# Optimization experiments

Hardware: AMD Instinct MI355X
Metric: run time of the kernel (lower is better)

Reference implementation:

```python
import jax, jax.numpy as jnp
import numpy as np

B, N, E, D, H = 1, 100000, 3200000, 16, 128
EPS = 1e-5


def _layer_norm(x, g, b):
    m = jnp.mean(x, axis=-1, keepdims=True)
    v = jnp.mean((x - m) ** 2, axis=-1, keepdims=True)
    return (x - m) * jax.lax.rsqrt(v + EPS) * g + b


def setup_inputs() -> dict:
    key = jax.random.key(0)
    ks = jax.random.split(key, 12)
    inp = {
        "nodes": jax.random.normal(ks[0], (B, N, D), dtype=jnp.float32),
        "edges": jax.random.randint(ks[1], (B, E, 2), 0, N, dtype=jnp.int32),
        "edge_weights": jax.random.uniform(ks[2], (B, E), dtype=jnp.float32),
    }
    dims = [(3 * D, H), (H, H), (H, H), (H, D)]
    for i, (din, dout) in enumerate(dims, start=1):
        inp[f"W{i}"] = jax.random.normal(ks[2 + i], (din, dout), dtype=jnp.float32) * (1.0 / np.sqrt(din))
        inp[f"b{i}"] = jnp.zeros((dout,), dtype=jnp.float32)
        inp[f"g{i}"] = jnp.ones((dout,), dtype=jnp.float32)
        inp[f"be{i}"] = jnp.zeros((dout,), dtype=jnp.float32)
    return inp


def reference(nodes, edges, edge_weights,
              W1, b1, g1, be1, W2, b2, g2, be2,
              W3, b3, g3, be3, W4, b4, g4, be4):
    src = edges[..., 0]  # [B,E]
    dst = edges[..., 1]
    w = edge_weights[..., None]  # [B,E,1]
    # edge-weighted endpoint features
    msg_in = jnp.take_along_axis(nodes, src[..., None], axis=1) * w   # [B,E,D]
    msg_out = jnp.take_along_axis(nodes, dst[..., None], axis=1) * w  # [B,E,D]
    # per-node sum aggregation (scatter-add over edge lists)
    b_idx = jnp.arange(B)[:, None]
    agg_in = jnp.zeros_like(nodes).at[b_idx, dst].add(msg_in)   # in-edges of node i
    agg_out = jnp.zeros_like(nodes).at[b_idx, src].add(msg_out)  # out-edges of node i
    x = jnp.concatenate([agg_in, agg_out, nodes], axis=2)  # [B,N,3D]
    x = jnp.tanh(_layer_norm(x @ W1 + b1, g1, be1))
    x = jnp.tanh(_layer_norm(x @ W2 + b2, g2, be2))
    x = jnp.tanh(_layer_norm(x @ W3 + b3, g3, be3))
    x = jnp.tanh(_layer_norm(x @ W4 + b4, g4, be4))
    return x
```

## Files before the change

### kernel.cpp

```cpp
#include <hip/hip_runtime.h>
#include <stdint.h>

#define DIM 16
#define HID 128
#define TN  64
#define ROWF 132
#define EPSF 1e-5f

#define FIX_SCALE 32768.0f
#define FIX_INV   (1.0f/32768.0f)
#define FIX_BIAS  (1 << 19)
#define FIX_MASK  0x7FFFFFF

__device__ __forceinline__ unsigned long long pack_term(float a, float b) {
    int ia = __float2int_rn(a * FIX_SCALE) + FIX_BIAS;
    int ib = __float2int_rn(b * FIX_SCALE) + FIX_BIAS;
    return (unsigned long long)(unsigned)ia
         | ((unsigned long long)(unsigned)ib << 27)
         | (1ULL << 54);
}

__device__ __forceinline__ float2 unpack_agg(unsigned long long v) {
    int cnt  = (int)(v >> 54);
    int f0   = (int)(v & FIX_MASK);
    int f1   = (int)((v >> 27) & FIX_MASK);
    int base = cnt << 19;
    return make_float2((float)(f0 - base) * FIX_INV,
                       (float)(f1 - base) * FIX_INV);
}

__device__ __forceinline__ float safe_tanh(float x) {
    float a = fabsf(x);
    float e = __expf(2.0f * a);
    float t = 1.0f - 2.0f / (e + 1.0f);
    return copysignf(t, x);
}

__global__ void __launch_bounds__(256) edge_scatter_kernel(
    const float* __restrict__ nodes, const int* __restrict__ edges,
    const float* __restrict__ ew,
    unsigned long long* __restrict__ agg_in,
    unsigned long long* __restrict__ agg_out, int nEdges)
{
    int gid = blockIdx.x * 256 + threadIdx.x;
    int e = gid >> 3;
    if (e >= nEdges) return;
    int p = gid & 7;
    int src = edges[2 * e];
    int dst = edges[2 * e + 1];
    float w  = ew[e];
    float2 vs = *(const float2*)(nodes + src * DIM + 2 * p);
    float2 vd = *(const float2*)(nodes + dst * DIM + 2 * p);
    atomicAdd(&agg_in [(size_t)dst * 8 + p], pack_term(vs.x * w, vs.y * w));
    atomicAdd(&agg_out[(size_t)src * 8 + p], pack_term(vd.x * w, vd.y * w));
}

template<int K>
__device__ __forceinline__ void dense_ln_tanh(
    const float* __restrict__ W, const float* __restrict__ bias,
    const float* __restrict__ g, const float* __restrict__ be,
    float (&X)[TN][ROWF], int tid)
{
    const int c0 = (tid & 31) * 4;
    const int n0 = (tid >> 5) * 8;
    float acc[8][4];
    {
        float4 bv = *(const float4*)(bias + c0);
        #pragma unroll
        for (int i = 0; i < 8; ++i) {
            acc[i][0] = bv.x; acc[i][1] = bv.y; acc[i][2] = bv.z; acc[i][3] = bv.w;
        }
    }

    #pragma unroll 2
    for (int k = 0; k < K; k += 4) {
        float xr[8][4];
        #pragma unroll
        for (int i = 0; i < 8; ++i) {
            float4 t = *(const float4*)&X[n0 + i][k];
            xr[i][0] = t.x; xr[i][1] = t.y; xr[i][2] = t.z; xr[i][3] = t.w;
        }
        float w[4][4];
        #pragma unroll
        for (int kk = 0; kk < 4; ++kk) {
            float4 t = *(const float4*)(W + (k + kk) * HID + c0);
            w[kk][0] = t.x; w[kk][1] = t.y; w[kk][2] = t.z; w[kk][3] = t.w;
        }
        #pragma unroll
        for (int kk = 0; kk < 4; ++kk)
            #pragma unroll
            for (int i = 0; i < 8; ++i)
                #pragma unroll
                for (int j = 0; j < 4; ++j) acc[i][j] += xr[i][kk] * w[kk][j];
    }

    float s[8], q[8];
    #pragma unroll
    for (int i = 0; i < 8; ++i) {
        s[i] = acc[i][0] + acc[i][1] + acc[i][2] + acc[i][3];
        q[i] = acc[i][0]*acc[i][0] + acc[i][1]*acc[i][1]
             + acc[i][2]*acc[i][2] + acc[i][3]*acc[i][3];
    }
    #pragma unroll
    for (int m = 1; m <= 16; m <<= 1) {
        #pragma unroll
        for (int i = 0; i < 8; ++i) {
            s[i] += __shfl_xor(s[i], m);
            q[i] += __shfl_xor(q[i], m);
        }
    }

    float4 gv  = *(const float4*)(g + c0);
    float4 bev = *(const float4*)(be + c0);
    float gr[4]  = {gv.x, gv.y, gv.z, gv.w};
    float ber[4] = {bev.x, bev.y, bev.z, bev.w};

    __syncthreads();
    #pragma unroll
    for (int i = 0; i < 8; ++i) {
        float mean = s[i] * (1.0f / HID);
        float var  = fmaxf(q[i] * (1.0f / HID) - mean * mean, 0.0f);
        float r = rsqrtf(var + EPSF);
        float o[4];
        #pragma unroll
        for (int j = 0; j < 4; ++j)
            o[j] = safe_tanh((acc[i][j] - mean) * r * gr[j] + ber[j]);
        *(float4*)&X[n0 + i][c0] = make_float4(o[0], o[1], o[2], o[3]);
    }
    __syncthreads();
}

__global__ void __launch_bounds__(256, 3) mlp_kernel(
    const unsigned long long* __restrict__ agg_in,
    const unsigned long long* __restrict__ agg_out,
    const float* __restrict__ nodes,
    const float* __restrict__ W1, const float* __restrict__ b1, const float* __restrict__ g1, const float* __restrict__ be1,
    const float* __restrict__ W2, const float* __restrict__ b2, const float* __restrict__ g2, const float* __restrict__ be2,
    const float* __restrict__ W3, const float* __restrict__ b3, const float* __restrict__ g3, const float* __restrict__ be3,
    const float* __restrict__ W4, const float* __restrict__ b4, const float* __restrict__ g4, const float* __restrict__ be4,
    float* __restrict__ out, int nNodes)
{
    __shared__ float X[TN][ROWF];

    const int tid = threadIdx.x;
    const int node0 = blockIdx.x * TN;

    for (int i = tid; i < TN * 16; i += 256) {
        int n = i >> 4, f = i & 15;
        int gn = node0 + n;
        float2 v = make_float2(0.f, 0.f);
        if (gn < nNodes) {
            unsigned long long pv = (f < 8)
                ? agg_in [(size_t)gn * 8 + f]
                : agg_out[(size_t)gn * 8 + (f - 8)];
            v = unpack_agg(pv);
        }
        *(float2*)&X[n][2 * f] = v;
    }
    for (int i = tid; i < TN * 4; i += 256) {
        int n = i >> 2, q = i & 3;
        int gn = node0 + n;
        float4 v = make_float4(0.f, 0.f, 0.f, 0.f);
        if (gn < nNodes) v = *(const float4*)(nodes + (size_t)gn * DIM + q * 4);
        *(float4*)&X[n][32 + q * 4] = v;
    }
    __syncthreads();

    dense_ln_tanh<48>(W1, b1, g1, be1, X, tid);
    dense_ln_tanh<128>(W2, b2, g2, be2, X, tid);
    dense_ln_tanh<128>(W3, b3, g3, be3, X, tid);

    {
        const int c2 = tid & 15;
        const int nb = tid >> 4;
        float a[4];
        {
            float bv = b4[c2];
            #pragma unroll
            for (int t = 0; t < 4; ++t) a[t] = bv;
        }
        #pragma unroll 2
        for (int k = 0; k < HID; k += 4) {
            float w[4];
            #pragma unroll
            for (int kk = 0; kk < 4; ++kk) w[kk] = W4[(k + kk) * DIM + c2];
            #pragma unroll
            for (int t = 0; t < 4; ++t) {
                float4 x = *(const float4*)&X[nb + 16 * t][k];
                a[t] += x.x * w[0] + x.y * w[1] + x.z * w[2] + x.w * w[3];
            }
        }
        float s[4], q[4];
        #pragma unroll
        for (int t = 0; t < 4; ++t) { s[t] = a[t]; q[t] = a[t] * a[t]; }
        #pragma unroll
        for (int m = 1; m <= 8; m <<= 1) {
            #pragma unroll
            for (int t = 0; t < 4; ++t) {
                s[t] += __shfl_xor(s[t], m);
                q[t] += __shfl_xor(q[t], m);
            }
        }
        float g4v = g4[c2], be4v = be4[c2];
        #pragma unroll
        for (int t = 0; t < 4; ++t) {
            int node = node0 + nb + 16 * t;
            if (node < nNodes) {
                float mean = s[t] * (1.0f / DIM);
                float var  = fmaxf(q[t] * (1.0f / DIM) - mean * mean, 0.0f);
                float o = safe_tanh((a[t] - mean) * rsqrtf(var + EPSF) * g4v + be4v);
                out[(size_t)node * DIM + c2] = o;
            }
        }
    }
}

extern "C" void kernel_launch(void* const* d_in, const int* in_sizes, int n_in,
                              void* d_out, int out_size, void* d_ws, size_t ws_size,
                              hipStream_t stream)
{
    const float* nodes = (const float*)d_in[0];
    const int*   edges = (const int*)d_in[1];
    const float* ew    = (const float*)d_in[2];
    const float *W1 = (const float*)d_in[3],  *b1 = (const float*)d_in[4],
                *g1 = (const float*)d_in[5],  *be1 = (const float*)d_in[6];
    const float *W2 = (const float*)d_in[7],  *b2 = (const float*)d_in[8],
                *g2 = (const float*)d_in[9],  *be2 = (const float*)d_in[10];
    const float *W3 = (const float*)d_in[11], *b3 = (const float*)d_in[12],
                *g3 = (const float*)d_in[13], *be3 = (const float*)d_in[14];
    const float *W4 = (const float*)d_in[15], *b4 = (const float*)d_in[16],
                *g4 = (const float*)d_in[17], *be4 = (const float*)d_in[18];

    const int N = in_sizes[0] / DIM;
    const int E = in_sizes[2];

    unsigned long long* agg_in  = (unsigned long long*)d_ws;
    unsigned long long* agg_out = agg_in + (size_t)N * 8;

    hipMemsetAsync(d_ws, 0, (size_t)2 * N * 8 * sizeof(unsigned long long), stream);

    long long ethreads = (long long)E * 8;
    int egrid = (int)((ethreads + 255) / 256);
    edge_scatter_kernel<<<egrid, 256, 0, stream>>>(nodes, edges, ew,
                                                   agg_in, agg_out, E);

    int mgrid = (N + TN - 1) / TN;
    mlp_kernel<<<mgrid, 256, 0, stream>>>(agg_in, agg_out, nodes,
        W1, b1, g1, be1, W2, b2, g2, be2, W3, b3, g3, be3, W4, b4, g4, be4,
        (float*)d_out, N);
}
```

Baseline: 541.1 us.

## Split edge scatter into separate in/out kernels and prefetch MLP weights

The single edge scatter kernel is split into two kernels, one accumulating incoming messages and one outgoing, so each pass writes into only one aggregation array. This may improve L2 locality of the atomics, at the cost of reading the edge list and weights twice plus an extra launch. Separately, the dense layer loop now software-prefetches the next four weight rows into registers while computing the current ones, to hide global load latency. The prefetch raises register pressure.

```diff
diff --git a/kernel.cpp b/kernel.cpp
--- a/kernel.cpp
+++ b/kernel.cpp
@@ -6,6 +6,8 @@
 #define TN  64
 #define ROWF 132
 #define EPSF 1e-5f
+
+typedef unsigned int u32;
 
 #define FIX_SCALE 32768.0f
 #define FIX_INV   (1.0f/32768.0f)
@@ -36,11 +38,10 @@
     return copysignf(t, x);
 }
 
-__global__ void __launch_bounds__(256) edge_scatter_kernel(
+__global__ void __launch_bounds__(256) scatter_in_kernel(
     const float* __restrict__ nodes, const int* __restrict__ edges,
     const float* __restrict__ ew,
-    unsigned long long* __restrict__ agg_in,
-    unsigned long long* __restrict__ agg_out, int nEdges)
+    unsigned long long* __restrict__ agg_in, int nEdges)
 {
     int gid = blockIdx.x * 256 + threadIdx.x;
     int e = gid >> 3;
@@ -50,8 +51,22 @@
     int dst = edges[2 * e + 1];
     float w  = ew[e];
     float2 vs = *(const float2*)(nodes + src * DIM + 2 * p);
+    atomicAdd(&agg_in[(size_t)dst * 8 + p], pack_term(vs.x * w, vs.y * w));
+}
+
+__global__ void __launch_bounds__(256) scatter_out_kernel(
+    const float* __restrict__ nodes, const int* __restrict__ edges,
+    const float* __restrict__ ew,
+    unsigned long long* __restrict__ agg_out, int nEdges)
+{
+    int gid = blockIdx.x * 256 + threadIdx.x;
+    int e = gid >> 3;
+    if (e >= nEdges) return;
+    int p = gid & 7;
+    int src = edges[2 * e];
+    int dst = edges[2 * e + 1];
+    float w  = ew[e];
     float2 vd = *(const float2*)(nodes + dst * DIM + 2 * p);
-    atomicAdd(&agg_in [(size_t)dst * 8 + p], pack_term(vs.x * w, vs.y * w));
     atomicAdd(&agg_out[(size_t)src * 8 + p], pack_term(vd.x * w, vd.y * w));
 }
 
@@ -72,26 +87,34 @@
         }
     }
 
-    #pragma unroll 2
+    float4 w[4];
+    #pragma unroll
+    for (int kk = 0; kk < 4; ++kk)
+        w[kk] = *(const float4*)(W + kk * HID + c0);
+
     for (int k = 0; k < K; k += 4) {
-        float xr[8][4];
+        float4 wn[4];
+        if (k + 4 < K) {
+            #pragma unroll
+            for (int kk = 0; kk < 4; ++kk)
+                wn[kk] = *(const float4*)(W + (k + 4 + kk) * HID + c0);
+        }
         #pragma unroll
         for (int i = 0; i < 8; ++i) {
-            float4 t = *(const float4*)&X[n0 + i][k];
-            xr[i][0] = t.x; xr[i][1] = t.y; xr[i][2] = t.z; xr[i][3] = t.w;
-        }
-        float w[4][4];
-        #pragma unroll
-        for (int kk = 0; kk < 4; ++kk) {
-            float4 t = *(const float4*)(W + (k + kk) * HID + c0);
-            w[kk][0] = t.x; w[kk][1] = t.y; w[kk][2] = t.z; w[kk][3] = t.w;
-        }
-        #pragma unroll
-        for (int kk = 0; kk < 4; ++kk)
-            #pragma unroll
-            for (int i = 0; i < 8; ++i)
-                #pragma unroll
-                for (int j = 0; j < 4; ++j) acc[i][j] += xr[i][kk] * w[kk][j];
+            float4 x = *(const float4*)&X[n0 + i][k];
+            float xr[4] = {x.x, x.y, x.z, x.w};
+            #pragma unroll
+            for (int kk = 0; kk < 4; ++kk) {
+                acc[i][0] += xr[kk] * w[kk].x;
+                acc[i][1] += xr[kk] * w[kk].y;
+                acc[i][2] += xr[kk] * w[kk].z;
+                acc[i][3] += xr[kk] * w[kk].w;
+            }
+        }
+        if (k + 4 < K) {
+            #pragma unroll
+            for (int kk = 0; kk < 4; ++kk) w[kk] = wn[kk];
+        }
     }
 
     float s[8], q[8];
@@ -241,8 +264,8 @@
 
     long long ethreads = (long long)E * 8;
     int egrid = (int)((ethreads + 255) / 256);
-    edge_scatter_kernel<<<egrid, 256, 0, stream>>>(nodes, edges, ew,
-                                                   agg_in, agg_out, E);
+    scatter_in_kernel <<<egrid, 256, 0, stream>>>(nodes, edges, ew, agg_in,  E);
+    scatter_out_kernel<<<egrid, 256, 0, stream>>>(nodes, edges, ew, agg_out, E);
 
     int mgrid = (N + TN - 1) / TN;
     mlp_kernel<<<mgrid, 256, 0, stream>>>(agg_in, agg_out, nodes,
```

Result: slower. 557.6 us (+3.1%).
